# Performance work log

Measured on AMD Instinct MI355X. Metric: run time of the kernel, lower is better.

The kernel has to match this reference:

```python
import jax, jax.numpy as jnp
import numpy as np

B, T, D = 4, 2048, 1024
H = 16
DK = D // H

def setup_inputs() -> dict:
    key = jax.random.key(0)
    k1, k2, k3, k4, k5 = jax.random.split(key, 5)
    s = 1.0 / np.sqrt(D)
    return {
        "x": jax.random.normal(k1, (B, T, D), dtype=jnp.float32),
        # torch Linear convention: weight [out, in], y = x @ W.T + b
        "W_qkv": jax.random.uniform(k2, (3 * D, D), jnp.float32, -s, s),
        "b_qkv": jax.random.uniform(k3, (3 * D,), jnp.float32, -s, s),
        "W_proj": jax.random.uniform(k4, (D, D), jnp.float32, -s, s),
        "b_proj": jax.random.uniform(k5, (D,), jnp.float32, -s, s),
    }

def reference(x, W_qkv, b_qkv, W_proj, b_proj):
    Bx, Tx, C = x.shape
    qkv = x @ W_qkv.T + b_qkv                      # [B,T,3D]
    qkv = qkv.reshape(Bx, Tx, 3, H, DK)
    qkv = jnp.transpose(qkv, (2, 0, 3, 1, 4))      # [3,B,H,T,dk]
    q, k, v = qkv[0], qkv[1], qkv[2]
    att = jnp.einsum('bhqd,bhkd->bhqk', q, k) / np.sqrt(DK)
    causal = jnp.tril(jnp.ones((Tx, Tx), dtype=bool))
    att = jnp.where(causal[None, None], att, -jnp.inf)
    att = jax.nn.softmax(att, axis=-1)
    out = jnp.einsum('bhqk,bhkd->bhqd', att, v)    # [B,H,T,dk]
    out = jnp.transpose(out, (0, 2, 1, 3)).reshape(Bx, Tx, C)
    return out @ W_proj.T + b_proj
```

## Files before the change

### kernel.cpp

```cpp
#include <hip/hip_runtime.h>

typedef unsigned short ushort_t;
typedef __attribute__((ext_vector_type(8))) short short8;
typedef __attribute__((ext_vector_type(4))) float f32x4;

#define DEV __device__ __forceinline__

constexpr int B_ = 4, T_ = 2048, D_ = 1024, H_ = 16;
constexpr int M_ = B_ * T_;
constexpr float LOG2E_ = 1.4426950408889634f;

DEV ushort_t f2bf(float f) {
  union { float f; unsigned u; } c; c.f = f;
  unsigned u = c.u;
  return (ushort_t)((u + 0x7fffu + ((u >> 16) & 1u)) >> 16);
}
DEV float bf2f(ushort_t b) {
  union { unsigned u; float f; } c; c.u = ((unsigned)b) << 16;
  return c.f;
}
DEV unsigned cvt_pk_bf16(float lo, float hi) {
  unsigned r;
  asm("v_cvt_pk_bf16_f32 %0, %1, %2" : "=v"(r) : "v"(lo), "v"(hi));
  return r;
}

DEV void gload_lds16(const void* g, void* l) {
  __builtin_amdgcn_global_load_lds(
      (const __attribute__((address_space(1))) void*)g,
      (__attribute__((address_space(3))) void*)l, 16, 0, 0);
}

__global__ void __launch_bounds__(256) f2bf3_kernel(
    const float* __restrict__ a, ushort_t* __restrict__ oa, int na4,
    const float* __restrict__ b, ushort_t* __restrict__ ob, int nb4,
    const float* __restrict__ c, ushort_t* __restrict__ oc, int nc4) {
  int stride = gridDim.x * blockDim.x;
  int ntot = na4 + nb4 + nc4;
  for (int i = blockIdx.x * blockDim.x + threadIdx.x; i < ntot; i += stride) {
    const float* src;
    ushort_t* dst;
    int j = i;
    if (j < na4) {
      src = a; dst = oa;
    } else if (j < na4 + nb4) {
      j -= na4; src = b; dst = ob;
    } else {
      j -= na4 + nb4; src = c; dst = oc;
    }
    float4 v = reinterpret_cast<const float4*>(src)[j];
    ushort4 o;
    o.x = f2bf(v.x); o.y = f2bf(v.y); o.z = f2bf(v.z); o.w = f2bf(v.w);
    reinterpret_cast<ushort4*>(dst)[j] = o;
  }
}

template <bool OUT_BF16>
__global__ void __launch_bounds__(512) gemm256(
    const ushort_t* __restrict__ A, const ushort_t* __restrict__ Bw,
    const float* __restrict__ bias, void* __restrict__ Cout,
    ushort_t* __restrict__ VT, int M, int N, int K, int ldc) {
  __shared__ __align__(16) ushort_t lA[3][256 * 64];
  __shared__ __align__(16) ushort_t lB[3][128 * 64];
  const int tid = threadIdx.x;
  const int lane = tid & 63;
  const int wid = tid >> 6;
  const int wm = wid >> 1, wn = wid & 1;
  const int r0 = lane & 15;
  const int p = lane >> 4;
  const int rg = p * 4;

  const int nbn = N >> 7;
  const int G = (M >> 8) * nbn;
  const int lin = blockIdx.x;
  const int cpx = G >> 3;
  const int swz = (lin & 7) * cpx + (lin >> 3);
  const int m0 = (swz / nbn) << 8;
  const int n0 = (swz % nbn) << 7;

  const int NKT = K >> 6;

  auto stage = [&](int kt, int slot) {
#pragma unroll
    for (int rnd = 0; rnd < 4; ++rnd) {
      int f = rnd * 4096 + tid * 8;
      int row = f >> 6;
      int sch = ((f >> 3) & 7) ^ (row & 7);
      gload_lds16(A + (size_t)(m0 + row) * K + kt * 64 + sch * 8,
                  &lA[slot][f]);
    }
#pragma unroll
    for (int rnd = 0; rnd < 2; ++rnd) {
      int f = rnd * 4096 + tid * 8;
      int row = f >> 6;
      int sch = ((f >> 3) & 7) ^ (row & 7);
      gload_lds16(Bw + (size_t)(n0 + row) * K + kt * 64 + sch * 8,
                  &lB[slot][f]);
    }
  };

  f32x4 acc[4][4] = {};

  stage(0, 0);
  stage(1, 1);

  for (int kt = 0; kt < NKT; ++kt) {
    int skt = kt + 2;
    if (skt >= NKT) skt -= NKT;
    stage(skt, (kt + 2) % 3);

    asm volatile("s_waitcnt vmcnt(12)" ::: "memory");
    __builtin_amdgcn_sched_barrier(0);
    asm volatile("s_barrier" ::: "memory");
    __builtin_amdgcn_sched_barrier(0);

    const ushort_t* bA = &lA[kt % 3][0];
    const ushort_t* bB = &lB[kt % 3][0];

    short8 aF[2][4], bF[2][4];
#pragma unroll
    for (int kc = 0; kc < 2; ++kc)
#pragma unroll
      for (int mi = 0; mi < 4; ++mi) {
        int row = wm * 64 + mi * 16 + r0;
        int ch = (kc * 4 + p) ^ (row & 7);
        aF[kc][mi] = *(const short8*)&bA[row * 64 + ch * 8];
      }
#pragma unroll
    for (int kc = 0; kc < 2; ++kc)
#pragma unroll
      for (int ni = 0; ni < 4; ++ni) {
        int row = wn * 64 + ni * 16 + r0;
        int ch = (kc * 4 + p) ^ (row & 7);
        bF[kc][ni] = *(const short8*)&bB[row * 64 + ch * 8];
      }

    __builtin_amdgcn_s_setprio(1);
#pragma unroll
    for (int kc = 0; kc < 2; ++kc)
#pragma unroll
      for (int mi = 0; mi < 4; ++mi)
#pragma unroll
        for (int ni = 0; ni < 4; ++ni)
          acc[mi][ni] = __builtin_amdgcn_mfma_f32_16x16x32_bf16(
              aF[kc][mi], bF[kc][ni], acc[mi][ni], 0, 0, 0);
    __builtin_amdgcn_s_setprio(0);

    asm volatile("s_barrier" ::: "memory");
    __builtin_amdgcn_sched_barrier(0);
  }

  const bool vpath = (VT != nullptr) && (n0 >= 2048);
  if (vpath) {
#pragma unroll
    for (int mi = 0; mi < 4; ++mi)
#pragma unroll
      for (int ni = 0; ni < 4; ++ni) {
        int n = n0 + wn * 64 + ni * 16 + r0;
        float bv = bias[n];
        int vcol = n - 2048;
        int hh = vcol >> 6, dd = vcol & 63;
        int m = m0 + wm * 64 + mi * 16 + rg;
        int bb = m >> 11, tt = m & 2047;
        ushort4 o;
        o.x = f2bf(acc[mi][ni][0] + bv);
        o.y = f2bf(acc[mi][ni][1] + bv);
        o.z = f2bf(acc[mi][ni][2] + bv);
        o.w = f2bf(acc[mi][ni][3] + bv);
        *reinterpret_cast<ushort4*>(
            &VT[((size_t)((bb << 4) + hh) * 64 + dd) * (size_t)T_ + tt]) = o;
      }
  } else {
#pragma unroll
    for (int mi = 0; mi < 4; ++mi)
#pragma unroll
      for (int ni = 0; ni < 4; ++ni) {
        int n = n0 + wn * 64 + ni * 16 + r0;
        float bv = bias[n];
#pragma unroll
        for (int r = 0; r < 4; ++r) {
          int m = m0 + wm * 64 + mi * 16 + rg + r;
          float v = acc[mi][ni][r] + bv;
          if (OUT_BF16)
            ((ushort_t*)Cout)[(size_t)m * ldc + n] = f2bf(v);
          else
            ((float*)Cout)[(size_t)m * ldc + n] = v;
        }
      }
  }
}

__global__ void __launch_bounds__(256, 4) attn_kernel(
    const ushort_t* __restrict__ qk, const ushort_t* __restrict__ Vt,
    ushort_t* __restrict__ O) {
  __shared__ __align__(16) ushort_t lK[2][64 * 64];
  __shared__ __align__(16) ushort_t lVT[2][64 * 64];
  __shared__ __align__(16) ushort_t lP[4][16 * 64];

  const int tid = threadIdx.x;
  const int lane = tid & 63;
  const int w = tid >> 6;
  const int r0 = lane & 15;
  const int p = lane >> 4;
  const int g8 = p * 8;
  const int rg = p * 4;

  const int lin = (int)blockIdx.y * 16 + (int)blockIdx.x;
  const int xcd = lin & 7;
  const int chunk = lin >> 3;
  const int bh = xcd * 8 + (chunk >> 4);
  const int pair = chunk & 15;

  const int b = bh >> 4, h = bh & 15;
  const float QSC = 0.125f * LOG2E_;

  const short8 bOne = {0x3F80, 0x3F80, 0x3F80, 0x3F80,
                       0x3F80, 0x3F80, 0x3F80, 0x3F80};

  ushort_t* lPw = &lP[w][0];

  const int f0 = tid * 8;
  const int row0 = f0 >> 6;
  const int lch0 = ((f0 >> 3) & 7) ^ (row0 & 7);
  const int f1 = 2048 + tid * 8;
  const int row1 = f1 >> 6;
  const int lch1 = ((f1 >> 3) & 7) ^ (row1 & 7);

  const int qb1 = pair;
  const int qb2 = 31 - pair;
  const int q1 = qb1 * 64 + w * 16;
  const int q2 = qb2 * 64 + w * 16;

  short8 aQ1[2], aQ2[2];
#pragma unroll
  for (int kc = 0; kc < 2; ++kc) {
    short8 raw1 = *(const short8*)(qk + (size_t)(b * T_ + q1 + r0) * 2048 +
                                   h * 64 + kc * 32 + g8);
    short8 raw2 = *(const short8*)(qk + (size_t)(b * T_ + q2 + r0) * 2048 +
                                   h * 64 + kc * 32 + g8);
    short8 s1, s2;
#pragma unroll
    for (int j = 0; j < 4; ++j) {
      unsigned pk1 = cvt_pk_bf16(bf2f((ushort_t)raw1[2 * j]) * QSC,
                                 bf2f((ushort_t)raw1[2 * j + 1]) * QSC);
      unsigned pk2 = cvt_pk_bf16(bf2f((ushort_t)raw2[2 * j]) * QSC,
                                 bf2f((ushort_t)raw2[2 * j + 1]) * QSC);
      s1[2 * j] = (short)(ushort_t)pk1;
      s1[2 * j + 1] = (short)(ushort_t)(pk1 >> 16);
      s2[2 * j] = (short)(ushort_t)pk2;
      s2[2 * j + 1] = (short)(ushort_t)(pk2 >> 16);
    }
    aQ1[kc] = s1;
    aQ2[kc] = s2;
  }

  f32x4 accO1[4] = {}, accO2[4] = {};
  f32x4 accL1 = {}, accL2 = {};

  {
    const ushort_t* kb = qk + (size_t)(b * T_) * 2048 + 1024 + h * 64;
    const ushort_t* vb = Vt + (size_t)bh * 64 * (size_t)T_;
    gload_lds16(kb + (size_t)row0 * 2048 + lch0 * 8, &lK[0][f0]);
    gload_lds16(kb + (size_t)row1 * 2048 + lch1 * 8, &lK[0][f1]);
    gload_lds16(vb + (size_t)row0 * T_ + lch0 * 8, &lVT[0][f0]);
    gload_lds16(vb + (size_t)row1 * T_ + lch1 * 8, &lVT[0][f1]);
  }
  int cur = 0;

  auto procPV = [&](f32x4* sA, const ushort_t* bufV, f32x4* accO,
                    f32x4& accL) {
#pragma unroll
    for (int ni = 0; ni < 4; ++ni) {
      float p0 = exp2f(sA[ni][0]);
      float p1 = exp2f(sA[ni][1]);
      float p2 = exp2f(sA[ni][2]);
      float p3 = exp2f(sA[ni][3]);
      unsigned lo = cvt_pk_bf16(p0, p1);
      unsigned hi = cvt_pk_bf16(p2, p3);
      int col = ni * 16 + r0;
#pragma unroll
      for (int r = 0; r < 4; ++r) {
        int rowp = rg + r;
        ushort_t hw = (r == 0)   ? (ushort_t)lo
                      : (r == 1) ? (ushort_t)(lo >> 16)
                      : (r == 2) ? (ushort_t)hi
                                 : (ushort_t)(hi >> 16);
        lPw[rowp * 64 + (col ^ ((rowp & 7) << 3))] = hw;
      }
    }
    __builtin_amdgcn_s_setprio(1);
#pragma unroll
    for (int kc = 0; kc < 2; ++kc) {
      int pch = (kc * 4 + p) ^ (r0 & 7);
      short8 aP = *(const short8*)&lPw[r0 * 64 + pch * 8];
      accL = __builtin_amdgcn_mfma_f32_16x16x32_bf16(aP, bOne, accL, 0, 0, 0);
#pragma unroll
      for (int ni = 0; ni < 4; ++ni) {
        int row = ni * 16 + r0;
        int ch = (kc * 4 + p) ^ (row & 7);
        short8 bV = *(const short8*)&bufV[row * 64 + ch * 8];
        accO[ni] =
            __builtin_amdgcn_mfma_f32_16x16x32_bf16(aP, bV, accO[ni], 0, 0, 0);
      }
    }
    __builtin_amdgcn_s_setprio(0);
  };

  for (int kt = 0; kt <= qb2; ++kt) {
    __syncthreads();

    if (kt < qb2) {
      const ushort_t* kb =
          qk + (size_t)(b * T_ + (kt + 1) * 64) * 2048 + 1024 + h * 64;
      const ushort_t* vb = Vt + (size_t)bh * 64 * (size_t)T_ + (kt + 1) * 64;
      ushort_t* dK = &lK[cur ^ 1][0];
      ushort_t* dV = &lVT[cur ^ 1][0];
      gload_lds16(kb + (size_t)row0 * 2048 + lch0 * 8, dK + f0);
      gload_lds16(kb + (size_t)row1 * 2048 + lch1 * 8, dK + f1);
      gload_lds16(vb + (size_t)row0 * T_ + lch0 * 8, dV + f0);
      gload_lds16(vb + (size_t)row1 * T_ + lch1 * 8, dV + f1);
    }

    const ushort_t* bufK = &lK[cur][0];
    const ushort_t* bufV = &lVT[cur][0];
    const bool act1 = (kt <= qb1);

    f32x4 sA2[4];
#pragma unroll
    for (int ni = 0; ni < 4; ++ni)
      sA2[ni] = f32x4{-16.f, -16.f, -16.f, -16.f};
    __builtin_amdgcn_s_setprio(1);
#pragma unroll
    for (int kc = 0; kc < 2; ++kc)
#pragma unroll
      for (int ni = 0; ni < 4; ++ni) {
        int row = ni * 16 + r0;
        int ch = (kc * 4 + p) ^ (row & 7);
        short8 bK = *(const short8*)&bufK[row * 64 + ch * 8];
        sA2[ni] =
            __builtin_amdgcn_mfma_f32_16x16x32_bf16(aQ2[kc], bK, sA2[ni], 0, 0, 0);
      }
    __builtin_amdgcn_s_setprio(0);
    if (kt == qb2) {
#pragma unroll
      for (int ni = 0; ni < 4; ++ni) {
        if (ni > w) {
#pragma unroll
          for (int r = 0; r < 4; ++r) sA2[ni][r] = -1e30f;
        } else if (ni == w) {
#pragma unroll
          for (int r = 0; r < 4; ++r)
            if (r0 > rg + r) sA2[ni][r] = -1e30f;
        }
      }
    }
    procPV(sA2, bufV, accO2, accL2);

    if (act1) {
      f32x4 sA1[4];
#pragma unroll
      for (int ni = 0; ni < 4; ++ni)
        sA1[ni] = f32x4{-16.f, -16.f, -16.f, -16.f};
      __builtin_amdgcn_s_setprio(1);
#pragma unroll
      for (int kc = 0; kc < 2; ++kc)
#pragma unroll
        for (int ni = 0; ni < 4; ++ni) {
          int row = ni * 16 + r0;
          int ch = (kc * 4 + p) ^ (row & 7);
          short8 bK = *(const short8*)&bufK[row * 64 + ch * 8];
          sA1[ni] = __builtin_amdgcn_mfma_f32_16x16x32_bf16(aQ1[kc], bK,
                                                            sA1[ni], 0, 0, 0);
        }
      __builtin_amdgcn_s_setprio(0);
      if (kt == qb1) {
#pragma unroll
        for (int ni = 0; ni < 4; ++ni) {
          if (ni > w) {
#pragma unroll
            for (int r = 0; r < 4; ++r) sA1[ni][r] = -1e30f;
          } else if (ni == w) {
#pragma unroll
            for (int r = 0; r < 4; ++r)
              if (r0 > rg + r) sA1[ni][r] = -1e30f;
          }
        }
      }
      procPV(sA1, bufV, accO1, accL1);
    }

    cur ^= 1;
  }

#pragma unroll
  for (int ni = 0; ni < 4; ++ni)
#pragma unroll
    for (int r = 0; r < 4; ++r) {
      int d = h * 64 + ni * 16 + r0;
      float v1 = accO1[ni][r] / accL1[r];
      float v2 = accO2[ni][r] / accL2[r];
      O[(size_t)(b * T_ + q1 + rg + r) * 1024 + d] = f2bf(v1);
      O[(size_t)(b * T_ + q2 + rg + r) * 1024 + d] = f2bf(v2);
    }
}

extern "C" void kernel_launch(void* const* d_in, const int* in_sizes, int n_in,
                              void* d_out, int out_size, void* d_ws, size_t ws_size,
                              hipStream_t stream) {
  const float* x = (const float*)d_in[0];
  const float* Wqkv = (const float*)d_in[1];
  const float* bqkv = (const float*)d_in[2];
  const float* Wproj = (const float*)d_in[3];
  const float* bproj = (const float*)d_in[4];
  float* out = (float*)d_out;

  ushort_t* xb = (ushort_t*)d_ws;
  ushort_t* wqkvb = xb + (size_t)M_ * D_;
  ushort_t* wprojb = wqkvb + (size_t)3 * D_ * D_;
  ushort_t* qkb = wprojb + (size_t)D_ * D_;
  ushort_t* Vt = qkb + (size_t)M_ * 2048;
  ushort_t* Ob = Vt + (size_t)M_ * D_;

  f2bf3_kernel<<<2048, 256, 0, stream>>>(
      x, xb, M_ * D_ / 4,
      Wqkv, wqkvb, 3 * D_ * D_ / 4,
      Wproj, wprojb, D_ * D_ / 4);

  gemm256<true><<<768, 512, 0, stream>>>(
      xb, wqkvb, bqkv, qkb, Vt, M_, 3 * D_, D_, 2048);

  attn_kernel<<<dim3(16, 64), 256, 0, stream>>>(qkb, Vt, Ob);

  gemm256<false><<<256, 512, 0, stream>>>(
      Ob, wprojb, bproj, out, nullptr, M_, D_, D_, D_);
}
```

Before: 184.4 us.

## Add 256x256 ping-pong GEMM with staged half-tile loads for QKV projection

Adds a new QKV GEMM kernel with a 256x256 block tile, twice the previous 256x128, which halves the grid to 384 blocks. It uses double-buffered LDS and splits each K-step into four quadrant MFMA phases, interleaving half-tile global->LDS loads with barriers and s_setprio so memory traffic overlaps compute. The larger tile raises data reuse per block, but it costs 128KB of LDS and more accumulator registers, and may lower occupancy.

```diff
diff --git a/kernel.cpp b/kernel.cpp
--- a/kernel.cpp
+++ b/kernel.cpp
@@ -55,6 +55,188 @@
   }
 }
 
+__global__ void __launch_bounds__(512) gemm8p(
+    const ushort_t* __restrict__ A, const ushort_t* __restrict__ Bw,
+    const float* __restrict__ bias, ushort_t* __restrict__ Cout,
+    ushort_t* __restrict__ VT, int M, int N, int K, int ldc) {
+  __shared__ __align__(16) ushort_t lA[2][256 * 64];
+  __shared__ __align__(16) ushort_t lB[2][256 * 64];
+  const int tid = threadIdx.x;
+  const int lane = tid & 63;
+  const int wid = tid >> 6;
+  const int wm = wid >> 2;
+  const int wn = wid & 3;
+  const int r0 = lane & 15;
+  const int p = lane >> 4;
+  const int rg = p * 4;
+
+  const int nbn = N >> 8;
+  const int G = (M >> 8) * nbn;
+  const int lin = blockIdx.x;
+  const int cpx = G >> 3;
+  const int swz = (lin & 7) * cpx + (lin >> 3);
+  const int m0 = (swz / nbn) << 8;
+  const int n0 = (swz % nbn) << 8;
+
+  const int NKT = K >> 6;
+
+  auto stageA = [&](int kt, int h, int slot) {
+#pragma unroll
+    for (int rnd = 0; rnd < 2; ++rnd) {
+      int f = rnd * 4096 + tid * 8;
+      int row = h * 128 + (f >> 6);
+      int sch = ((f >> 3) & 7) ^ (row & 7);
+      gload_lds16(A + (size_t)(m0 + row) * K + kt * 64 + sch * 8,
+                  &lA[slot][h * 8192 + f]);
+    }
+  };
+  auto stageB = [&](int kt, int h, int slot) {
+#pragma unroll
+    for (int rnd = 0; rnd < 2; ++rnd) {
+      int f = rnd * 4096 + tid * 8;
+      int row = h * 128 + (f >> 6);
+      int sch = ((f >> 3) & 7) ^ (row & 7);
+      gload_lds16(Bw + (size_t)(n0 + row) * K + kt * 64 + sch * 8,
+                  &lB[slot][h * 8192 + f]);
+    }
+  };
+
+  f32x4 acc[8][4] = {};
+
+  stageA(0, 0, 0);
+  stageB(0, 0, 0);
+  stageA(0, 1, 0);
+  stageB(0, 1, 0);
+
+  for (int kt = 0; kt < NKT; ++kt) {
+    const int cur = kt & 1, nxt = cur ^ 1;
+    const bool hn = (kt + 1 < NKT);
+    const ushort_t* bA = &lA[cur][0];
+    const ushort_t* bB = &lB[cur][0];
+    const int chbase = (r0 & 7);
+
+    short8 aQ0[2][4], aQ1[2][4], bF0[2][2], bF1[2][2];
+
+    if (hn) {
+      stageA(kt + 1, 0, nxt);
+      asm volatile("s_waitcnt vmcnt(2)" ::: "memory");
+    } else {
+      asm volatile("s_waitcnt vmcnt(0)" ::: "memory");
+    }
+    asm volatile("s_barrier" ::: "memory");
+#pragma unroll
+    for (int kc = 0; kc < 2; ++kc) {
+      int ch = (kc * 4 + p) ^ chbase;
+#pragma unroll
+      for (int mi = 0; mi < 4; ++mi) {
+        int row = wm * 128 + mi * 16 + r0;
+        aQ0[kc][mi] = *(const short8*)&bA[row * 64 + ch * 8];
+      }
+#pragma unroll
+      for (int ni = 0; ni < 2; ++ni) {
+        int row = wn * 64 + ni * 16 + r0;
+        bF0[kc][ni] = *(const short8*)&bB[row * 64 + ch * 8];
+      }
+    }
+    __builtin_amdgcn_s_setprio(1);
+#pragma unroll
+    for (int kc = 0; kc < 2; ++kc)
+#pragma unroll
+      for (int mi = 0; mi < 4; ++mi)
+#pragma unroll
+        for (int ni = 0; ni < 2; ++ni)
+          acc[mi][ni] = __builtin_amdgcn_mfma_f32_16x16x32_bf16(
+              aQ0[kc][mi], bF0[kc][ni], acc[mi][ni], 0, 0, 0);
+    __builtin_amdgcn_s_setprio(0);
+    asm volatile("s_barrier" ::: "memory");
+
+    if (hn) stageB(kt + 1, 0, nxt);
+#pragma unroll
+    for (int kc = 0; kc < 2; ++kc) {
+      int ch = (kc * 4 + p) ^ chbase;
+#pragma unroll
+      for (int mi = 0; mi < 4; ++mi) {
+        int row = wm * 128 + 64 + mi * 16 + r0;
+        aQ1[kc][mi] = *(const short8*)&bA[row * 64 + ch * 8];
+      }
+    }
+    __builtin_amdgcn_s_setprio(1);
+#pragma unroll
+    for (int kc = 0; kc < 2; ++kc)
+#pragma unroll
+      for (int mi = 0; mi < 4; ++mi)
+#pragma unroll
+        for (int ni = 0; ni < 2; ++ni)
+          acc[4 + mi][ni] = __builtin_amdgcn_mfma_f32_16x16x32_bf16(
+              aQ1[kc][mi], bF0[kc][ni], acc[4 + mi][ni], 0, 0, 0);
+    __builtin_amdgcn_s_setprio(0);
+    asm volatile("s_barrier" ::: "memory");
+
+    if (hn) stageA(kt + 1, 1, nxt);
+#pragma unroll
+    for (int kc = 0; kc < 2; ++kc) {
+      int ch = (kc * 4 + p) ^ chbase;
+#pragma unroll
+      for (int ni = 0; ni < 2; ++ni) {
+        int row = wn * 64 + 32 + ni * 16 + r0;
+        bF1[kc][ni] = *(const short8*)&bB[row * 64 + ch * 8];
+      }
+    }
+    __builtin_amdgcn_s_setprio(1);
+#pragma unroll
+    for (int kc = 0; kc < 2; ++kc)
+#pragma unroll
+      for (int mi = 0; mi < 4; ++mi)
+#pragma unroll
+        for (int ni = 0; ni < 2; ++ni)
+          acc[4 + mi][2 + ni] = __builtin_amdgcn_mfma_f32_16x16x32_bf16(
+              aQ1[kc][mi], bF1[kc][ni], acc[4 + mi][2 + ni], 0, 0, 0);
+    __builtin_amdgcn_s_setprio(0);
+    asm volatile("s_barrier" ::: "memory");
+
+    if (hn) stageB(kt + 1, 1, nxt);
+    __builtin_amdgcn_s_setprio(1);
+#pragma unroll
+    for (int kc = 0; kc < 2; ++kc)
+#pragma unroll
+      for (int mi = 0; mi < 4; ++mi)
+#pragma unroll
+        for (int ni = 0; ni < 2; ++ni)
+          acc[mi][2 + ni] = __builtin_amdgcn_mfma_f32_16x16x32_bf16(
+              aQ0[kc][mi], bF1[kc][ni], acc[mi][2 + ni], 0, 0, 0);
+    __builtin_amdgcn_s_setprio(0);
+    asm volatile("s_barrier" ::: "memory");
+  }
+
+#pragma unroll
+  for (int ai = 0; ai < 8; ++ai) {
+    int mh = ai >> 2, mi = ai & 3;
+    int m = m0 + wm * 128 + mh * 64 + mi * 16 + rg;
+#pragma unroll
+    for (int bj = 0; bj < 4; ++bj) {
+      int nh = bj >> 1, ni = bj & 1;
+      int n = n0 + wn * 64 + nh * 32 + ni * 16 + r0;
+      float bv = bias[n];
+      if (n >= 2048) {
+        int vcol = n - 2048;
+        int hh = vcol >> 6, dd = vcol & 63;
+        int bb = m >> 11, tt = m & 2047;
+        ushort4 o;
+        o.x = f2bf(acc[ai][bj][0] + bv);
+        o.y = f2bf(acc[ai][bj][1] + bv);
+        o.z = f2bf(acc[ai][bj][2] + bv);
+        o.w = f2bf(acc[ai][bj][3] + bv);
+        *reinterpret_cast<ushort4*>(
+            &VT[((size_t)((bb << 4) + hh) * 64 + dd) * (size_t)T_ + tt]) = o;
+      } else {
+#pragma unroll
+        for (int r = 0; r < 4; ++r)
+          Cout[(size_t)(m + r) * ldc + n] = f2bf(acc[ai][bj][r] + bv);
+      }
+    }
+  }
+}
+
 template <bool OUT_BF16>
 __global__ void __launch_bounds__(512) gemm256(
     const ushort_t* __restrict__ A, const ushort_t* __restrict__ Bw,
@@ -426,7 +608,7 @@
       Wqkv, wqkvb, 3 * D_ * D_ / 4,
       Wproj, wprojb, D_ * D_ / 4);
 
-  gemm256<true><<<768, 512, 0, stream>>>(
+  gemm8p<<<384, 512, 0, stream>>>(
       xb, wqkvb, bqkv, qkb, Vt, M_, 3 * D_, D_, 2048);
 
   attn_kernel<<<dim3(16, 64), 256, 0, stream>>>(qkb, Vt, Ob);
```

New measurement: 193.2 us. 4.8% more time.

## Use 256x256 tiles for the QKV GEMM and share K fragment loads in attention

Applied to the files above, without the earlier changes.

Adds a new QKV GEMM kernel with 256x256 output tiles, double-buffered LDS and 8 waves each computing 128x64, launched as 384 blocks instead of 768 with 256x128 tiles. The larger tile is meant to cut global and LDS traffic per FLOP. In exchange it raises register pressure (32 accumulators per wave) and reduces grid parallelism to fewer than two waves of blocks on the device. Separately, the attention kernel now computes QK^T for both query tiles inside one loop, so each K fragment read from LDS feeds two MFMAs instead of being loaded twice.

```diff
diff --git a/kernel.cpp b/kernel.cpp
--- a/kernel.cpp
+++ b/kernel.cpp
@@ -55,11 +55,128 @@
   }
 }
 
+__global__ void __launch_bounds__(512) gemm256sq(
+    const ushort_t* __restrict__ A, const ushort_t* __restrict__ Bw,
+    const float* __restrict__ bias, ushort_t* __restrict__ Cout,
+    ushort_t* __restrict__ VT, int M, int N, int K, int ldc) {
+  __shared__ __align__(16) ushort_t lA[2][256 * 64];
+  __shared__ __align__(16) ushort_t lB[2][256 * 64];
+  const int tid = threadIdx.x;
+  const int lane = tid & 63;
+  const int wid = tid >> 6;
+  const int wm = wid >> 2;
+  const int wn = wid & 3;
+  const int r0 = lane & 15;
+  const int p = lane >> 4;
+  const int rg = p * 4;
+
+  const int nbn = N >> 8;
+  const int G = (M >> 8) * nbn;
+  const int lin = blockIdx.x;
+  const int cpx = G >> 3;
+  const int swz = (lin & 7) * cpx + (lin >> 3);
+  const int m0 = (swz / nbn) << 8;
+  const int n0 = (swz % nbn) << 8;
+
+  const int NKT = K >> 6;
+
+  auto stage = [&](int kt, int slot) {
+#pragma unroll
+    for (int rnd = 0; rnd < 4; ++rnd) {
+      int f = rnd * 4096 + tid * 8;
+      int row = f >> 6;
+      int sch = ((f >> 3) & 7) ^ (row & 7);
+      gload_lds16(A + (size_t)(m0 + row) * K + kt * 64 + sch * 8,
+                  &lA[slot][f]);
+    }
+#pragma unroll
+    for (int rnd = 0; rnd < 4; ++rnd) {
+      int f = rnd * 4096 + tid * 8;
+      int row = f >> 6;
+      int sch = ((f >> 3) & 7) ^ (row & 7);
+      gload_lds16(Bw + (size_t)(n0 + row) * K + kt * 64 + sch * 8,
+                  &lB[slot][f]);
+    }
+  };
+
+  f32x4 acc[8][4] = {};
+
+  stage(0, 0);
+
+  for (int kt = 0; kt < NKT; ++kt) {
+    const int cur = kt & 1, nxt = cur ^ 1;
+    int skt = kt + 1;
+    if (skt >= NKT) skt -= NKT;
+    stage(skt, nxt);
+
+    asm volatile("s_waitcnt vmcnt(8)" ::: "memory");
+    __builtin_amdgcn_sched_barrier(0);
+    asm volatile("s_barrier" ::: "memory");
+    __builtin_amdgcn_sched_barrier(0);
+
+    const ushort_t* bA = &lA[cur][0];
+    const ushort_t* bB = &lB[cur][0];
+
+#pragma unroll
+    for (int kc = 0; kc < 2; ++kc) {
+      const int ch = (kc * 4 + p) ^ (r0 & 7);
+      short8 aF[8], bF[4];
+#pragma unroll
+      for (int mi = 0; mi < 8; ++mi) {
+        int row = wm * 128 + mi * 16 + r0;
+        aF[mi] = *(const short8*)&bA[row * 64 + ch * 8];
+      }
+#pragma unroll
+      for (int ni = 0; ni < 4; ++ni) {
+        int row = wn * 64 + ni * 16 + r0;
+        bF[ni] = *(const short8*)&bB[row * 64 + ch * 8];
+      }
+      __builtin_amdgcn_s_setprio(1);
+#pragma unroll
+      for (int mi = 0; mi < 8; ++mi)
+#pragma unroll
+        for (int ni = 0; ni < 4; ++ni)
+          acc[mi][ni] = __builtin_amdgcn_mfma_f32_16x16x32_bf16(
+              aF[mi], bF[ni], acc[mi][ni], 0, 0, 0);
+      __builtin_amdgcn_s_setprio(0);
+    }
+
+    asm volatile("s_barrier" ::: "memory");
+    __builtin_amdgcn_sched_barrier(0);
+  }
+
+#pragma unroll
+  for (int mi = 0; mi < 8; ++mi) {
+    int m = m0 + wm * 128 + mi * 16 + rg;
+#pragma unroll
+    for (int ni = 0; ni < 4; ++ni) {
+      int n = n0 + wn * 64 + ni * 16 + r0;
+      float bv = bias[n];
+      if (n >= 2048) {
+        int vcol = n - 2048;
+        int hh = vcol >> 6, dd = vcol & 63;
+        int bb = m >> 11, tt = m & 2047;
+        ushort4 o;
+        o.x = f2bf(acc[mi][ni][0] + bv);
+        o.y = f2bf(acc[mi][ni][1] + bv);
+        o.z = f2bf(acc[mi][ni][2] + bv);
+        o.w = f2bf(acc[mi][ni][3] + bv);
+        *reinterpret_cast<ushort4*>(
+            &VT[((size_t)((bb << 4) + hh) * 64 + dd) * (size_t)T_ + tt]) = o;
+      } else {
+#pragma unroll
+        for (int r = 0; r < 4; ++r)
+          Cout[(size_t)(m + r) * ldc + n] = f2bf(acc[mi][ni][r] + bv);
+      }
+    }
+  }
+}
+
 template <bool OUT_BF16>
 __global__ void __launch_bounds__(512) gemm256(
     const ushort_t* __restrict__ A, const ushort_t* __restrict__ Bw,
     const float* __restrict__ bias, void* __restrict__ Cout,
-    ushort_t* __restrict__ VT, int M, int N, int K, int ldc) {
+    int M, int N, int K, int ldc) {
   __shared__ __align__(16) ushort_t lA[3][256 * 64];
   __shared__ __align__(16) ushort_t lB[3][128 * 64];
   const int tid = threadIdx.x;
@@ -150,44 +267,22 @@
     __builtin_amdgcn_sched_barrier(0);
   }
 
-  const bool vpath = (VT != nullptr) && (n0 >= 2048);
-  if (vpath) {
-#pragma unroll
-    for (int mi = 0; mi < 4; ++mi)
-#pragma unroll
-      for (int ni = 0; ni < 4; ++ni) {
-        int n = n0 + wn * 64 + ni * 16 + r0;
-        float bv = bias[n];
-        int vcol = n - 2048;
-        int hh = vcol >> 6, dd = vcol & 63;
-        int m = m0 + wm * 64 + mi * 16 + rg;
-        int bb = m >> 11, tt = m & 2047;
-        ushort4 o;
-        o.x = f2bf(acc[mi][ni][0] + bv);
-        o.y = f2bf(acc[mi][ni][1] + bv);
-        o.z = f2bf(acc[mi][ni][2] + bv);
-        o.w = f2bf(acc[mi][ni][3] + bv);
-        *reinterpret_cast<ushort4*>(
-            &VT[((size_t)((bb << 4) + hh) * 64 + dd) * (size_t)T_ + tt]) = o;
-      }
-  } else {
-#pragma unroll
-    for (int mi = 0; mi < 4; ++mi)
-#pragma unroll
-      for (int ni = 0; ni < 4; ++ni) {
-        int n = n0 + wn * 64 + ni * 16 + r0;
-        float bv = bias[n];
-#pragma unroll
-        for (int r = 0; r < 4; ++r) {
-          int m = m0 + wm * 64 + mi * 16 + rg + r;
-          float v = acc[mi][ni][r] + bv;
-          if (OUT_BF16)
-            ((ushort_t*)Cout)[(size_t)m * ldc + n] = f2bf(v);
-          else
-            ((float*)Cout)[(size_t)m * ldc + n] = v;
-        }
-      }
-  }
+#pragma unroll
+  for (int mi = 0; mi < 4; ++mi)
+#pragma unroll
+    for (int ni = 0; ni < 4; ++ni) {
+      int n = n0 + wn * 64 + ni * 16 + r0;
+      float bv = bias[n];
+#pragma unroll
+      for (int r = 0; r < 4; ++r) {
+        int m = m0 + wm * 64 + mi * 16 + rg + r;
+        float v = acc[mi][ni][r] + bv;
+        if (OUT_BF16)
+          ((ushort_t*)Cout)[(size_t)m * ldc + n] = f2bf(v);
+        else
+          ((float*)Cout)[(size_t)m * ldc + n] = v;
+      }
+    }
 }
 
 __global__ void __launch_bounds__(256, 4) attn_kernel(
@@ -325,10 +420,12 @@
     const ushort_t* bufV = &lVT[cur][0];
     const bool act1 = (kt <= qb1);
 
-    f32x4 sA2[4];
-#pragma unroll
-    for (int ni = 0; ni < 4; ++ni)
+    f32x4 sA1[4], sA2[4];
+#pragma unroll
+    for (int ni = 0; ni < 4; ++ni) {
+      sA1[ni] = f32x4{-16.f, -16.f, -16.f, -16.f};
       sA2[ni] = f32x4{-16.f, -16.f, -16.f, -16.f};
+    }
     __builtin_amdgcn_s_setprio(1);
 #pragma unroll
     for (int kc = 0; kc < 2; ++kc)
@@ -339,8 +436,12 @@
         short8 bK = *(const short8*)&bufK[row * 64 + ch * 8];
         sA2[ni] =
             __builtin_amdgcn_mfma_f32_16x16x32_bf16(aQ2[kc], bK, sA2[ni], 0, 0, 0);
+        if (act1)
+          sA1[ni] = __builtin_amdgcn_mfma_f32_16x16x32_bf16(aQ1[kc], bK,
+                                                            sA1[ni], 0, 0, 0);
       }
     __builtin_amdgcn_s_setprio(0);
+
     if (kt == qb2) {
 #pragma unroll
       for (int ni = 0; ni < 4; ++ni) {
@@ -357,22 +458,6 @@
     procPV(sA2, bufV, accO2, accL2);
 
     if (act1) {
-      f32x4 sA1[4];
-#pragma unroll
-      for (int ni = 0; ni < 4; ++ni)
-        sA1[ni] = f32x4{-16.f, -16.f, -16.f, -16.f};
-      __builtin_amdgcn_s_setprio(1);
-#pragma unroll
-      for (int kc = 0; kc < 2; ++kc)
-#pragma unroll
-        for (int ni = 0; ni < 4; ++ni) {
-          int row = ni * 16 + r0;
-          int ch = (kc * 4 + p) ^ (row & 7);
-          short8 bK = *(const short8*)&bufK[row * 64 + ch * 8];
-          sA1[ni] = __builtin_amdgcn_mfma_f32_16x16x32_bf16(aQ1[kc], bK,
-                                                            sA1[ni], 0, 0, 0);
-        }
-      __builtin_amdgcn_s_setprio(0);
       if (kt == qb1) {
 #pragma unroll
         for (int ni = 0; ni < 4; ++ni) {
@@ -426,11 +511,11 @@
       Wqkv, wqkvb, 3 * D_ * D_ / 4,
       Wproj, wprojb, D_ * D_ / 4);
 
-  gemm256<true><<<768, 512, 0, stream>>>(
+  gemm256sq<<<384, 512, 0, stream>>>(
       xb, wqkvb, bqkv, qkb, Vt, M_, 3 * D_, D_, 2048);
 
   attn_kernel<<<dim3(16, 64), 256, 0, stream>>>(qkb, Vt, Ob);
 
   gemm256<false><<<256, 512, 0, stream>>>(
-      Ob, wprojb, bproj, out, nullptr, M_, D_, D_, D_);
-}
+      Ob, wprojb, bproj, out, M_, D_, D_, D_);
+}
```

Result: slower. 414.7 us (+125.0%).

## Single-buffer V tile in attention with split vmcnt waits and barriers

Applied to the files above, without the earlier changes.

Replaces the double-buffered V^T shared-memory tile with a single buffer loaded at the start of each key tile. Explicit vmcnt waits and raw s_barriers let QK^T scores and the P writes proceed while V is still in flight. The P write and the PV multiply are split so the V wait sits between them. This reduces LDS footprint and changes synchronisation, but V load latency may become exposed, and a redundant K load is issued on the final iteration.

```diff
diff --git a/kernel.cpp b/kernel.cpp
--- a/kernel.cpp
+++ b/kernel.cpp
@@ -194,7 +194,7 @@
     const ushort_t* __restrict__ qk, const ushort_t* __restrict__ Vt,
     ushort_t* __restrict__ O) {
   __shared__ __align__(16) ushort_t lK[2][64 * 64];
-  __shared__ __align__(16) ushort_t lVT[2][64 * 64];
+  __shared__ __align__(16) ushort_t lV[64 * 64];
   __shared__ __align__(16) ushort_t lP[4][16 * 64];
 
   const int tid = threadIdx.x;
@@ -257,18 +257,14 @@
   f32x4 accO1[4] = {}, accO2[4] = {};
   f32x4 accL1 = {}, accL2 = {};
 
-  {
-    const ushort_t* kb = qk + (size_t)(b * T_) * 2048 + 1024 + h * 64;
-    const ushort_t* vb = Vt + (size_t)bh * 64 * (size_t)T_;
-    gload_lds16(kb + (size_t)row0 * 2048 + lch0 * 8, &lK[0][f0]);
-    gload_lds16(kb + (size_t)row1 * 2048 + lch1 * 8, &lK[0][f1]);
-    gload_lds16(vb + (size_t)row0 * T_ + lch0 * 8, &lVT[0][f0]);
-    gload_lds16(vb + (size_t)row1 * T_ + lch1 * 8, &lVT[0][f1]);
-  }
+  const ushort_t* kbase = qk + (size_t)(b * T_) * 2048 + 1024 + h * 64;
+  const ushort_t* vbase = Vt + (size_t)bh * 64 * (size_t)T_;
+
+  gload_lds16(kbase + (size_t)row0 * 2048 + lch0 * 8, &lK[0][f0]);
+  gload_lds16(kbase + (size_t)row1 * 2048 + lch1 * 8, &lK[0][f1]);
   int cur = 0;
 
-  auto procPV = [&](f32x4* sA, const ushort_t* bufV, f32x4* accO,
-                    f32x4& accL) {
+  auto writeP = [&](f32x4* sA) {
 #pragma unroll
     for (int ni = 0; ni < 4; ++ni) {
       float p0 = exp2f(sA[ni][0]);
@@ -288,6 +284,8 @@
         lPw[rowp * 64 + (col ^ ((rowp & 7) << 3))] = hw;
       }
     }
+  };
+  auto doPV = [&](f32x4* accO, f32x4& accL) {
     __builtin_amdgcn_s_setprio(1);
 #pragma unroll
     for (int kc = 0; kc < 2; ++kc) {
@@ -298,7 +296,7 @@
       for (int ni = 0; ni < 4; ++ni) {
         int row = ni * 16 + r0;
         int ch = (kc * 4 + p) ^ (row & 7);
-        short8 bV = *(const short8*)&bufV[row * 64 + ch * 8];
+        short8 bV = *(const short8*)&lV[row * 64 + ch * 8];
         accO[ni] =
             __builtin_amdgcn_mfma_f32_16x16x32_bf16(aP, bV, accO[ni], 0, 0, 0);
       }
@@ -307,22 +305,26 @@
   };
 
   for (int kt = 0; kt <= qb2; ++kt) {
-    __syncthreads();
-
-    if (kt < qb2) {
-      const ushort_t* kb =
-          qk + (size_t)(b * T_ + (kt + 1) * 64) * 2048 + 1024 + h * 64;
-      const ushort_t* vb = Vt + (size_t)bh * 64 * (size_t)T_ + (kt + 1) * 64;
+    asm volatile("s_barrier" ::: "memory");
+    __builtin_amdgcn_sched_barrier(0);
+
+    {
+      const ushort_t* vb = vbase + kt * 64;
+      gload_lds16(vb + (size_t)row0 * T_ + lch0 * 8, &lV[f0]);
+      gload_lds16(vb + (size_t)row1 * T_ + lch1 * 8, &lV[f1]);
+      int nk = (kt < qb2) ? (kt + 1) : 0;
+      const ushort_t* kb = kbase + (size_t)nk * 64 * 2048;
       ushort_t* dK = &lK[cur ^ 1][0];
-      ushort_t* dV = &lVT[cur ^ 1][0];
       gload_lds16(kb + (size_t)row0 * 2048 + lch0 * 8, dK + f0);
       gload_lds16(kb + (size_t)row1 * 2048 + lch1 * 8, dK + f1);
-      gload_lds16(vb + (size_t)row0 * T_ + lch0 * 8, dV + f0);
-      gload_lds16(vb + (size_t)row1 * T_ + lch1 * 8, dV + f1);
-    }
+    }
+
+    asm volatile("s_waitcnt vmcnt(4)" ::: "memory");
+    __builtin_amdgcn_sched_barrier(0);
+    asm volatile("s_barrier" ::: "memory");
+    __builtin_amdgcn_sched_barrier(0);
 
     const ushort_t* bufK = &lK[cur][0];
-    const ushort_t* bufV = &lVT[cur][0];
     const bool act1 = (kt <= qb1);
 
     f32x4 sA2[4];
@@ -354,7 +356,14 @@
         }
       }
     }
-    procPV(sA2, bufV, accO2, accL2);
+    writeP(sA2);
+
+    asm volatile("s_waitcnt vmcnt(2)" ::: "memory");
+    __builtin_amdgcn_sched_barrier(0);
+    asm volatile("s_barrier" ::: "memory");
+    __builtin_amdgcn_sched_barrier(0);
+
+    doPV(accO2, accL2);
 
     if (act1) {
       f32x4 sA1[4];
@@ -386,11 +395,14 @@
           }
         }
       }
-      procPV(sA1, bufV, accO1, accL1);
+      writeP(sA1);
+      doPV(accO1, accL1);
     }
 
     cur ^= 1;
   }
+
+  asm volatile("s_waitcnt vmcnt(0)" ::: "memory");
 
 #pragma unroll
   for (int ni = 0; ni < 4; ++ni)
```

Measured after the change: 186.9 us. Within noise of the previous version (+1.4%).
